# Optimization experiments

Measured on AMD Instinct MI355X. Metric: run time of the kernel, lower is better.

## Reference

```python
import jax, jax.numpy as jnp
import numpy as np

H = 128; W = 128; WH = 8; WW = 8; SH = 4; SW = 4
DIM = 512; HEADS = 16; HD = DIM // HEADS; HIDDEN = 2048
NH = H // WH; NW = W // WW; NWIN = NH * NW; WL = WH * WW
EPS = 1e-5
SCALE = HD ** -0.5


def _rel_pos_index():
    # Swin-style relative position index, static (WL, WL) int table
    coords = np.stack(np.meshgrid(np.arange(WH), np.arange(WW), indexing='ij')).reshape(2, -1)
    rel = (coords[:, :, None] - coords[:, None, :]).transpose(1, 2, 0)  # (WL, WL, 2)
    rel[:, :, 0] += WH - 1
    rel[:, :, 1] += WW - 1
    rel[:, :, 0] *= 2 * WW - 1
    return rel.sum(-1)  # (WL, WL), values in [0, (2WH-1)(2WW-1))


def _shift_attn_mask():
    # static shifted-window attention mask, (NWIN, WL, WL)
    m = np.zeros((H, W))
    cnt = 0
    for hs in (slice(0, -WH), slice(-WH, -SH), slice(-SH, None)):
        for ws in (slice(0, -WW), slice(-WW, -SW), slice(-SW, None)):
            m[hs, ws] = cnt
            cnt += 1
    mw = m.reshape(NH, WH, NW, WW).transpose(0, 2, 1, 3).reshape(NWIN, WL)
    am = mw[:, None, :] - mw[:, :, None]
    return np.where(am != 0, -100.0, 0.0).astype(np.float32)


_RPI = _rel_pos_index()
_MASK = _shift_attn_mask()


def _layernorm(x, w, b):
    mu = x.mean(-1, keepdims=True)
    var = ((x - mu) ** 2).mean(-1, keepdims=True)
    return (x - mu) / jnp.sqrt(var + EPS) * w + b


def _win_part(x):  # (H, W, D) -> (NWIN, WL, D)
    return x.reshape(NH, WH, NW, WW, DIM).transpose(0, 2, 1, 3, 4).reshape(NWIN, WL, DIM)


def _win_rev(w):  # (NWIN, WL, D) -> (H, W, D)
    return w.reshape(NH, NW, WH, WW, DIM).transpose(0, 2, 1, 3, 4).reshape(H, W, DIM)


def setup_inputs() -> dict:
    key = jax.random.key(0)
    ks = jax.random.split(key, 8)
    s = 0.02
    return {
        'x': jax.random.normal(ks[0], (H * W, DIM), dtype=jnp.float32),
        'ln1_w': jnp.ones((DIM,), jnp.float32),
        'ln1_b': jnp.zeros((DIM,), jnp.float32),
        'ln2_w': jnp.ones((DIM,), jnp.float32),
        'ln2_b': jnp.zeros((DIM,), jnp.float32),
        'qkv_w': jax.random.normal(ks[1], (3 * DIM, DIM), dtype=jnp.float32) * s,
        'qkv_b': jnp.zeros((3 * DIM,), jnp.float32),
        'proj_w': jax.random.normal(ks[2], (DIM, DIM), dtype=jnp.float32) * s,
        'proj_b': jnp.zeros((DIM,), jnp.float32),
        'rpb': jax.random.normal(ks[3], ((2 * WH - 1) * (2 * WW - 1), HEADS), dtype=jnp.float32) * s,
        'mlp_w1': jax.random.normal(ks[4], (HIDDEN, DIM), dtype=jnp.float32) * s,
        'mlp_b1': jnp.zeros((HIDDEN,), jnp.float32),
        'mlp_w2': jax.random.normal(ks[5], (DIM, HIDDEN), dtype=jnp.float32) * s,
        'mlp_b2': jnp.zeros((DIM,), jnp.float32),
    }


def reference(x, ln1_w, ln1_b, ln2_w, ln2_b, qkv_w, qkv_b, proj_w, proj_b, rpb,
              mlp_w1, mlp_b1, mlp_w2, mlp_b2):
    skip = x
    h = _layernorm(x, ln1_w, ln1_b).reshape(H, W, DIM)
    # cyclic shift + window partition
    h = jnp.roll(h, shift=(-SH, -SW), axis=(0, 1))
    xw = _win_part(h)  # (NWIN, WL, DIM)
    # windowed multi-head self-attention (equinox Linear: y = W @ x + b)
    qkv = jnp.einsum('nld,ed->nle', xw, qkv_w) + qkv_b
    q, k, v = [t.reshape(NWIN, WL, HEADS, HD).transpose(0, 2, 1, 3)
               for t in jnp.split(qkv, 3, axis=-1)]  # each (NWIN, HEADS, WL, HD)
    attn = jnp.einsum('nhqd,nhkd->nhqk', q * SCALE, k)
    bias = rpb[_RPI.reshape(-1)].reshape(WL, WL, HEADS).transpose(2, 0, 1)  # (HEADS, WL, WL)
    attn = attn + bias[None] + jnp.asarray(_MASK)[:, None]
    attn = jax.nn.softmax(attn, axis=-1)
    out = jnp.einsum('nhqk,nhkd->nhqd', attn, v).transpose(0, 2, 1, 3).reshape(NWIN, WL, DIM)
    out = jnp.einsum('nld,ed->nle', out, proj_w) + proj_b
    # window reverse + reverse cyclic shift
    h = jnp.roll(_win_rev(out), shift=(SH, SW), axis=(0, 1)).reshape(H * W, DIM)
    h = skip + h  # residual (drop_path is Identity at rate 0)
    # FFN branch (note: original code does x = x + drop_path(x), i.e. 2*mlp(norm2(.)))
    h = _layernorm(h, ln2_w, ln2_b)
    m = jax.nn.gelu(jnp.einsum('ld,ed->le', h, mlp_w1) + mlp_b1)
    m = jnp.einsum('le,de->ld', m, mlp_w2) + mlp_b2
    return m + m
```

## Files before the change

### kernel.cpp

```cpp
#include <hip/hip_runtime.h>
#include <hip/hip_bf16.h>
#include <stdint.h>

#define TOK   16384
#define DIMM  512
#define NHEAD 16
#define HDIM  32
#define HID   2048
#define NWIN  256
#define WLEN  64
#define EPSV  1e-5f
#define SCL   0.17677669529663687f

typedef __hip_bfloat16 bf16;
typedef __attribute__((ext_vector_type(8))) __bf16 bf16x8;
typedef __attribute__((ext_vector_type(4))) float f32x4;

__device__ __forceinline__ int remap_row(int r){
  int win = r >> 6, l = r & 63;
  int gh = ((win >> 4) << 3) + (l >> 3);
  int gw = ((win & 15) << 3) + (l & 7);
  int oh = (gh + 4) & 127, ow = (gw + 4) & 127;
  return (oh << 7) + ow;
}

__device__ __forceinline__ int region_of(int win, int l){
  int gh = ((win >> 4) << 3) + (l >> 3);
  int gw = ((win & 15) << 3) + (l & 7);
  int rh = (gh < 120) ? 0 : ((gh < 124) ? 1 : 2);
  int rw = (gw < 120) ? 0 : ((gw < 124) ? 1 : 2);
  return rh * 3 + rw;
}

__device__ __forceinline__ void gl_lds16(const bf16* g, bf16* l){
  __builtin_amdgcn_global_load_lds((const __attribute__((address_space(1))) void*)g,
                                   (__attribute__((address_space(3))) void*)l, 16, 0, 0);
}

__global__ __launch_bounds__(256) void convert_w(const float* __restrict__ a,
                                                 const float* __restrict__ b,
                                                 const float* __restrict__ c,
                                                 const float* __restrict__ d,
                                                 bf16* __restrict__ dst){
  int e = (blockIdx.x * 256 + threadIdx.x) * 4;
  float4 v;
  if (e < 786432)        v = *(const float4*)(a + e);
  else if (e < 1048576)  v = *(const float4*)(b + (e - 786432));
  else if (e < 2097152)  v = *(const float4*)(c + (e - 1048576));
  else                   v = *(const float4*)(d + (e - 2097152));
  union { bf16 h[4]; int2 q; } u;
  u.h[0] = __float2bfloat16(v.x); u.h[1] = __float2bfloat16(v.y);
  u.h[2] = __float2bfloat16(v.z); u.h[3] = __float2bfloat16(v.w);
  *(int2*)(dst + e) = u.q;
}

template<bool REMAP>
__global__ __launch_bounds__(256) void ln_kernel(const float* __restrict__ in,
    const float* __restrict__ w, const float* __restrict__ b, bf16* __restrict__ outp)
{
  const int wave = threadIdx.x >> 6, lane = threadIdx.x & 63;
  const int r = blockIdx.x * 4 + wave;
  const int src = REMAP ? remap_row(r) : r;
  const float4* row = (const float4*)(in + (size_t)src * DIMM);
  float4 v0 = row[lane*2], v1 = row[lane*2 + 1];
  float sm = v0.x+v0.y+v0.z+v0.w + v1.x+v1.y+v1.z+v1.w;
  float sq = v0.x*v0.x+v0.y*v0.y+v0.z*v0.z+v0.w*v0.w
           + v1.x*v1.x+v1.y*v1.y+v1.z*v1.z+v1.w*v1.w;
  #pragma unroll
  for (int off = 1; off < 64; off <<= 1){
    sm += __shfl_xor(sm, off);
    sq += __shfl_xor(sq, off);
  }
  const float mean = sm * (1.f/512.f);
  const float rstd = rsqrtf(sq*(1.f/512.f) - mean*mean + EPSV);
  const float4* wp = (const float4*)w; const float4* bp = (const float4*)b;
  float4 w0 = wp[lane*2], w1 = wp[lane*2+1], b0 = bp[lane*2], b1 = bp[lane*2+1];
  union { bf16 h[8]; int4 q; } u;
  u.h[0] = __float2bfloat16((v0.x-mean)*rstd*w0.x + b0.x);
  u.h[1] = __float2bfloat16((v0.y-mean)*rstd*w0.y + b0.y);
  u.h[2] = __float2bfloat16((v0.z-mean)*rstd*w0.z + b0.z);
  u.h[3] = __float2bfloat16((v0.w-mean)*rstd*w0.w + b0.w);
  u.h[4] = __float2bfloat16((v1.x-mean)*rstd*w1.x + b1.x);
  u.h[5] = __float2bfloat16((v1.y-mean)*rstd*w1.y + b1.y);
  u.h[6] = __float2bfloat16((v1.z-mean)*rstd*w1.z + b1.z);
  u.h[7] = __float2bfloat16((v1.w-mean)*rstd*w1.w + b1.w);
  *(int4*)(outp + (size_t)r*DIMM + lane*8) = u.q;
}

#define M_QKV  0
#define M_PROJ 1
#define M_MLP1 2
#define M_MLP2 3

template<int MODE, int K>
__global__ __launch_bounds__(256) void gemm_bt(const bf16* __restrict__ A,
    const bf16* __restrict__ Wt, const float* __restrict__ bias,
    bf16* __restrict__ out_b, float* __restrict__ out_f, const float* __restrict__ skip)
{
  __shared__ bf16 lsA[2][128*32];
  __shared__ bf16 lsB[2][128*32];
  const int tid = threadIdx.x, wave = tid >> 6, lane = tid & 63;
  const int lrow = lane & 15, lgrp = lane >> 4;
  const int m0 = blockIdx.x * 128, n0 = blockIdx.y * 128;
  const int wr = (wave >> 1) * 64, wc = (wave & 1) * 64;

  f32x4 acc[4][4] = {};

  const bf16* Abase = A  + (size_t)m0 * K;
  const bf16* Bbase = Wt + (size_t)n0 * K;
  const int srow = tid >> 2;
  const int scol = (tid & 3) * 8;

  #define STAGE(kt, bf) { \
    gl_lds16(Abase + (size_t)(srow)      * K + (kt) + scol, lsA[bf] + wave*512); \
    gl_lds16(Abase + (size_t)(srow + 64) * K + (kt) + scol, lsA[bf] + 2048 + wave*512); \
    gl_lds16(Bbase + (size_t)(srow)      * K + (kt) + scol, lsB[bf] + wave*512); \
    gl_lds16(Bbase + (size_t)(srow + 64) * K + (kt) + scol, lsB[bf] + 2048 + wave*512); \
  }

  STAGE(0, 0);
  __syncthreads();
  int cur = 0;
  for (int kt = 0; kt < K; kt += 32){
    if (kt + 32 < K) STAGE(kt + 32, cur ^ 1);
    bf16x8 af[4], bfv[4];
    #pragma unroll
    for (int i = 0; i < 4; i++){
      af[i]  = *(const bf16x8*)(lsA[cur] + (wr + i*16 + lrow)*32 + lgrp*8);
      bfv[i] = *(const bf16x8*)(lsB[cur] + (wc + i*16 + lrow)*32 + lgrp*8);
    }
    #pragma unroll
    for (int i = 0; i < 4; i++)
      #pragma unroll
      for (int j = 0; j < 4; j++)
        acc[i][j] = __builtin_amdgcn_mfma_f32_16x16x32_bf16(af[i], bfv[j], acc[i][j], 0, 0, 0);
    __syncthreads();
    cur ^= 1;
  }
  #undef STAGE

  #pragma unroll
  for (int i = 0; i < 4; i++){
    #pragma unroll
    for (int j = 0; j < 4; j++){
      const int col   = n0 + wc + j*16 + lrow;
      const int row_b = m0 + wr + i*16 + lgrp*4;
      const float bv = bias[col];
      #pragma unroll
      for (int rr = 0; rr < 4; rr++){
        const int row = row_b + rr;
        float v = acc[i][j][rr] + bv;
        if constexpr (MODE == M_QKV){
          const int t = col >> 9, rem = col & 511;
          const int head = rem >> 5, hd = rem & 31;
          const int win = row >> 6, l = row & 63;
          out_b[(size_t)t * (TOK*DIMM) + ((size_t)(win*NHEAD + head)*WLEN + l)*HDIM + hd]
              = __float2bfloat16(v);
        } else if constexpr (MODE == M_PROJ){
          const int o = remap_row(row);
          out_f[(size_t)o*DIMM + col] = v + skip[(size_t)o*DIMM + col];
        } else if constexpr (MODE == M_MLP1){
          const float u = 1.5957691216057308f * (v + 0.044715f*v*v*v);
          const float g = v * (1.0f / (1.0f + __expf(-u)));
          out_b[(size_t)row*HID + col] = __float2bfloat16(g);
        } else {
          out_f[(size_t)row*DIMM + col] = 2.f * v;
        }
      }
    }
  }
}

__global__ __launch_bounds__(256) void attn_kernel(const bf16* __restrict__ qkv,
    const float* __restrict__ rpb, bf16* __restrict__ outp)
{
  __shared__ bf16 Pl[4][64][72];
  const int wave = threadIdx.x >> 6, lane = threadIdx.x & 63;
  const int lrow = lane & 15, lgrp = lane >> 4;
  const int wh = blockIdx.x * 4 + wave;
  const int win = wh >> 4, head = wh & 15;
  const bf16* qb = qkv + (size_t)wh * (WLEN*HDIM);
  const bf16* kb = qb + (size_t)TOK * DIMM;
  const bf16* vb = kb + (size_t)TOK * DIMM;

  bf16x8 aq[4], ak[4];
  #pragma unroll
  for (int i = 0; i < 4; i++){
    aq[i] = *(const bf16x8*)(qb + (i*16 + lrow)*HDIM + lgrp*8);
    ak[i] = *(const bf16x8*)(kb + (i*16 + lrow)*HDIM + lgrp*8);
  }
  f32x4 s[4][4] = {};
  #pragma unroll
  for (int i = 0; i < 4; i++)
    #pragma unroll
    for (int j = 0; j < 4; j++)
      s[i][j] = __builtin_amdgcn_mfma_f32_16x16x32_bf16(aq[i], ak[j], s[i][j], 0, 0, 0);

  #pragma unroll
  for (int i = 0; i < 4; i++){
    #pragma unroll
    for (int rr = 0; rr < 4; rr++){
      const int srow = i*16 + lgrp*4 + rr;
      const int rq = region_of(win, srow);
      float vals[4]; float mx = -1e30f;
      #pragma unroll
      for (int j = 0; j < 4; j++){
        const int scol = j*16 + lrow;
        const int idx = ((srow>>3) - (scol>>3) + 7)*15 + ((srow&7) - (scol&7) + 7);
        float v = s[i][j][rr]*SCL + rpb[idx*NHEAD + head];
        if (region_of(win, scol) != rq) v -= 100.f;
        vals[j] = v; mx = fmaxf(mx, v);
      }
      mx = fmaxf(mx, __shfl_xor(mx, 1));
      mx = fmaxf(mx, __shfl_xor(mx, 2));
      mx = fmaxf(mx, __shfl_xor(mx, 4));
      mx = fmaxf(mx, __shfl_xor(mx, 8));
      float sum = 0.f;
      #pragma unroll
      for (int j = 0; j < 4; j++){ vals[j] = __expf(vals[j] - mx); sum += vals[j]; }
      sum += __shfl_xor(sum, 1); sum += __shfl_xor(sum, 2);
      sum += __shfl_xor(sum, 4); sum += __shfl_xor(sum, 8);
      const float rs = 1.f / sum;
      #pragma unroll
      for (int j = 0; j < 4; j++)
        Pl[wave][srow][j*16 + lrow] = __float2bfloat16(vals[j] * rs);
    }
  }

  f32x4 o[4][2] = {};
  const __bf16* vraw = (const __bf16*)vb;
  #pragma unroll
  for (int st = 0; st < 2; st++){
    bf16x8 pa[4];
    #pragma unroll
    for (int i = 0; i < 4; i++)
      pa[i] = *(const bf16x8*)(&Pl[wave][i*16 + lrow][st*32 + lgrp*8]);
    bf16x8 bv[2];
    #pragma unroll
    for (int j = 0; j < 2; j++){
      #pragma unroll
      for (int jj = 0; jj < 8; jj++)
        bv[j][jj] = vraw[(size_t)(st*32 + lgrp*8 + jj)*HDIM + j*16 + lrow];
    }
    #pragma unroll
    for (int i = 0; i < 4; i++)
      #pragma unroll
      for (int j = 0; j < 2; j++)
        o[i][j] = __builtin_amdgcn_mfma_f32_16x16x32_bf16(pa[i], bv[j], o[i][j], 0, 0, 0);
  }
  bf16* orow = outp + (size_t)win * WLEN * DIMM + head * HDIM;
  #pragma unroll
  for (int i = 0; i < 4; i++)
    #pragma unroll
    for (int j = 0; j < 2; j++)
      #pragma unroll
      for (int rr = 0; rr < 4; rr++){
        const int l = i*16 + lgrp*4 + rr;
        orow[(size_t)l * DIMM + j*16 + lrow] = __float2bfloat16(o[i][j][rr]);
      }
}

extern "C" void kernel_launch(void* const* d_in, const int* in_sizes, int n_in,
                              void* d_out, int out_size, void* d_ws, size_t ws_size,
                              hipStream_t stream) {
  const float* x     = (const float*)d_in[0];
  const float* ln1w  = (const float*)d_in[1];
  const float* ln1b  = (const float*)d_in[2];
  const float* ln2w  = (const float*)d_in[3];
  const float* ln2b  = (const float*)d_in[4];
  const float* qkvw  = (const float*)d_in[5];
  const float* qkvbi = (const float*)d_in[6];
  const float* projw = (const float*)d_in[7];
  const float* projb = (const float*)d_in[8];
  const float* rpb   = (const float*)d_in[9];
  const float* m1w   = (const float*)d_in[10];
  const float* m1b   = (const float*)d_in[11];
  const float* m2w   = (const float*)d_in[12];
  const float* m2b   = (const float*)d_in[13];

  bf16* wqkv  = (bf16*)d_ws;
  bf16* wproj = wqkv + 786432;
  bf16* wm1   = wproj + 262144;
  bf16* wm2   = wm1 + 1048576;
  bf16* xw    = wm2 + 1048576;
  float* hbuf = (float*)(xw + 8388608);
  bf16* qkvb  = (bf16*)(hbuf + 8388608);
  bf16* attno = qkvb + 3*(size_t)8388608;
  bf16* m1buf = qkvb;
  bf16* h2    = xw;

  convert_w<<<3072, 256, 0, stream>>>(qkvw, projw, m1w, m2w, wqkv);
  ln_kernel<true><<<4096, 256, 0, stream>>>(x, ln1w, ln1b, xw);
  { dim3 g(TOK/128, 1536/128);
    gemm_bt<M_QKV, 512><<<g, 256, 0, stream>>>(xw, wqkv, qkvbi, qkvb, nullptr, nullptr); }
  attn_kernel<<<1024, 256, 0, stream>>>(qkvb, rpb, attno);
  { dim3 g(TOK/128, 512/128);
    gemm_bt<M_PROJ, 512><<<g, 256, 0, stream>>>(attno, wproj, projb, nullptr, hbuf, x); }
  ln_kernel<false><<<4096, 256, 0, stream>>>(hbuf, ln2w, ln2b, h2);
  { dim3 g(TOK/128, 2048/128);
    gemm_bt<M_MLP1, 512><<<g, 256, 0, stream>>>(h2, wm1, m1b, m1buf, nullptr, nullptr); }
  { dim3 g(TOK/128, 512/128);
    gemm_bt<M_MLP2, 2048><<<g, 256, 0, stream>>>(m1buf, wm2, m2b, nullptr, (float*)d_out, nullptr); }
}
```

Before: 227.6 us.

## Add 256x256 eight-wave pipelined GEMM for QKV and MLP projections

Introduces a new GEMM kernel with 256x256 tiles, 512 threads (8 waves), double-buffered LDS staging via direct global-to-LDS loads, and an interleaved schedule that overlaps MFMA quadrants with LDS reads and next-tile prefetch using explicit barriers and priority hints. The QKV, MLP1 and MLP2 GEMMs now use it, while the proj GEMM keeps the old kernel, whose epilogue is trimmed to proj and generic modes. The larger tile raises arithmetic intensity and cuts global traffic. In exchange it uses 128KB of dynamic LDS and launches fewer blocks, which may hurt occupancy and tail balance, especially for MLP2 with 128 blocks.

```diff
diff --git a/kernel.cpp b/kernel.cpp
--- a/kernel.cpp
+++ b/kernel.cpp
@@ -150,15 +150,117 @@
       for (int rr = 0; rr < 4; rr++){
         const int row = row_b + rr;
         float v = acc[i][j][rr] + bv;
+        if constexpr (MODE == M_PROJ){
+          const int o = remap_row(row);
+          out_f[(size_t)o*DIMM + col] = v + skip[(size_t)o*DIMM + col];
+        } else {
+          out_f[(size_t)row*DIMM + col] = v;
+        }
+      }
+    }
+  }
+}
+
+__device__ __forceinline__ void stage_ht(const bf16* __restrict__ P, int Kdim,
+                                         int grow0, bf16* lbase, int tid, int kt){
+  const int r = tid >> 3, c = (tid & 7) * 8;
+  const bf16* g = P + (size_t)(grow0 + r) * Kdim + kt * 64 + c;
+  bf16* l = lbase + r * 64 + c;
+  gl_lds16(g, l);
+  gl_lds16(g + (size_t)64 * Kdim, l + 4096);
+}
+
+template<int MODE, int K>
+__global__ __launch_bounds__(512, 2) void gemm8_bt(const bf16* __restrict__ A,
+    const bf16* __restrict__ Wt, const float* __restrict__ bias,
+    bf16* __restrict__ out_b, float* __restrict__ out_f)
+{
+  constexpr int NT = K / 64;
+  extern __shared__ bf16 lds[];
+  bf16* As = lds;
+  bf16* Bs = lds + 32768;
+  const int tid = threadIdx.x;
+  const int ln = tid & 63, wv = tid >> 6;
+  const int lrow = ln & 15, lgrp = ln >> 4;
+  const int wm = wv >> 2, wn = wv & 3;
+  const int m0 = blockIdx.x * 256, n0 = blockIdx.y * 256;
+
+  f32x4 acc[8][4] = {};
+  bf16x8 aA[4][2], bB0[2][2], bB1[2][2];
+
+  #define LDA(MH) { _Pragma("unroll") for (int mf = 0; mf < 4; mf++) \
+    _Pragma("unroll") for (int ks = 0; ks < 2; ks++) \
+      aA[mf][ks] = *(const bf16x8*)(As + s*16384 + (wm*128 + (MH)*64 + mf*16 + lrow)*64 + ks*32 + lgrp*8); }
+  #define LDB(DST, NH) { _Pragma("unroll") for (int nf = 0; nf < 2; nf++) \
+    _Pragma("unroll") for (int ks = 0; ks < 2; ks++) \
+      DST[nf][ks] = *(const bf16x8*)(Bs + s*16384 + (wn*64 + (NH)*32 + nf*16 + lrow)*64 + ks*32 + lgrp*8); }
+  #define QUAD(BARR, IM0, JN0) { _Pragma("unroll") for (int ks = 0; ks < 2; ks++) \
+    _Pragma("unroll") for (int mf = 0; mf < 4; mf++) \
+      _Pragma("unroll") for (int nf = 0; nf < 2; nf++) \
+        acc[(IM0)+mf][(JN0)+nf] = __builtin_amdgcn_mfma_f32_16x16x32_bf16(aA[mf][ks], BARR[nf][ks], acc[(IM0)+mf][(JN0)+nf], 0, 0, 0); }
+  #define SBAR() { __builtin_amdgcn_sched_barrier(0); __builtin_amdgcn_s_barrier(); __builtin_amdgcn_sched_barrier(0); }
+  #define LGKM0() { asm volatile("s_waitcnt lgkmcnt(0)" ::: "memory"); __builtin_amdgcn_sched_barrier(0); }
+
+  stage_ht(A,  K, m0,       As,        tid, 0);
+  stage_ht(Wt, K, n0,       Bs,        tid, 0);
+  stage_ht(Wt, K, n0 + 128, Bs + 8192, tid, 0);
+  stage_ht(A,  K, m0 + 128, As + 8192, tid, 0);
+  asm volatile("s_waitcnt vmcnt(0)" ::: "memory");
+  SBAR();
+  stage_ht(Wt, K, n0,       Bs + 16384,        tid, 1);
+  stage_ht(A,  K, m0,       As + 16384,        tid, 1);
+  stage_ht(Wt, K, n0 + 128, Bs + 16384 + 8192, tid, 1);
+
+  for (int t = 0; t < NT; ++t){
+    const int s = t & 1;
+    const int sx = s ^ 1;
+    LDA(0); LDB(bB0, 0);
+    if (t + 1 < NT) stage_ht(A, K, m0 + 128, As + sx*16384 + 8192, tid, t + 1);
+    SBAR(); LGKM0();
+    __builtin_amdgcn_s_setprio(1); QUAD(bB0, 0, 0); __builtin_amdgcn_s_setprio(0);
+    SBAR();
+    LDB(bB1, 1);
+    SBAR(); LGKM0();
+    __builtin_amdgcn_s_setprio(1); QUAD(bB1, 0, 2); __builtin_amdgcn_s_setprio(0);
+    SBAR();
+    LDA(1);
+    if (t + 2 < NT) stage_ht(Wt, K, n0, Bs + s*16384, tid, t + 2);
+    SBAR(); LGKM0();
+    __builtin_amdgcn_s_setprio(1); QUAD(bB1, 4, 2); __builtin_amdgcn_s_setprio(0);
+    SBAR();
+    if (t + 2 < NT){
+      stage_ht(A,  K, m0,       As + s*16384,        tid, t + 2);
+      stage_ht(Wt, K, n0 + 128, Bs + s*16384 + 8192, tid, t + 2);
+    }
+    SBAR();
+    __builtin_amdgcn_s_setprio(1); QUAD(bB0, 4, 0); __builtin_amdgcn_s_setprio(0);
+    if (t == NT - 2)      { asm volatile("s_waitcnt vmcnt(0)" ::: "memory"); }
+    else if (t < NT - 2)  { asm volatile("s_waitcnt vmcnt(6)" ::: "memory"); }
+    SBAR();
+  }
+  #undef LDA
+  #undef LDB
+  #undef QUAD
+  #undef SBAR
+  #undef LGKM0
+
+  #pragma unroll
+  for (int im = 0; im < 8; im++){
+    #pragma unroll
+    for (int jn = 0; jn < 4; jn++){
+      const int col = n0 + wn*64 + (jn >> 1)*32 + (jn & 1)*16 + lrow;
+      const int row_b = m0 + wm*128 + (im >> 2)*64 + (im & 3)*16 + lgrp*4;
+      const float bv = bias[col];
+      #pragma unroll
+      for (int rr = 0; rr < 4; rr++){
+        const int row = row_b + rr;
+        float v = acc[im][jn][rr] + bv;
         if constexpr (MODE == M_QKV){
           const int t = col >> 9, rem = col & 511;
           const int head = rem >> 5, hd = rem & 31;
           const int win = row >> 6, l = row & 63;
           out_b[(size_t)t * (TOK*DIMM) + ((size_t)(win*NHEAD + head)*WLEN + l)*HDIM + hd]
               = __float2bfloat16(v);
-        } else if constexpr (MODE == M_PROJ){
-          const int o = remap_row(row);
-          out_f[(size_t)o*DIMM + col] = v + skip[(size_t)o*DIMM + col];
         } else if constexpr (MODE == M_MLP1){
           const float u = 1.5957691216057308f * (v + 0.044715f*v*v*v);
           const float g = v * (1.0f / (1.0f + __expf(-u)));
@@ -289,16 +391,23 @@
   bf16* m1buf = qkvb;
   bf16* h2    = xw;
 
+  hipFuncSetAttribute((const void*)&gemm8_bt<M_QKV, 512>,
+                      hipFuncAttributeMaxDynamicSharedMemorySize, 131072);
+  hipFuncSetAttribute((const void*)&gemm8_bt<M_MLP1, 512>,
+                      hipFuncAttributeMaxDynamicSharedMemorySize, 131072);
+  hipFuncSetAttribute((const void*)&gemm8_bt<M_MLP2, 2048>,
+                      hipFuncAttributeMaxDynamicSharedMemorySize, 131072);
+
   convert_w<<<3072, 256, 0, stream>>>(qkvw, projw, m1w, m2w, wqkv);
   ln_kernel<true><<<4096, 256, 0, stream>>>(x, ln1w, ln1b, xw);
-  { dim3 g(TOK/128, 1536/128);
-    gemm_bt<M_QKV, 512><<<g, 256, 0, stream>>>(xw, wqkv, qkvbi, qkvb, nullptr, nullptr); }
+  { dim3 g(TOK/256, 1536/256);
+    gemm8_bt<M_QKV, 512><<<g, 512, 131072, stream>>>(xw, wqkv, qkvbi, qkvb, nullptr); }
   attn_kernel<<<1024, 256, 0, stream>>>(qkvb, rpb, attno);
   { dim3 g(TOK/128, 512/128);
     gemm_bt<M_PROJ, 512><<<g, 256, 0, stream>>>(attno, wproj, projb, nullptr, hbuf, x); }
   ln_kernel<false><<<4096, 256, 0, stream>>>(hbuf, ln2w, ln2b, h2);
-  { dim3 g(TOK/128, 2048/128);
-    gemm_bt<M_MLP1, 512><<<g, 256, 0, stream>>>(h2, wm1, m1b, m1buf, nullptr, nullptr); }
-  { dim3 g(TOK/128, 512/128);
-    gemm_bt<M_MLP2, 2048><<<g, 256, 0, stream>>>(m1buf, wm2, m2b, nullptr, (float*)d_out, nullptr); }
-}
+  { dim3 g(TOK/256, 2048/256);
+    gemm8_bt<M_MLP1, 512><<<g, 512, 131072, stream>>>(h2, wm1, m1b, m1buf, nullptr); }
+  { dim3 g(TOK/256, 512/256);
+    gemm8_bt<M_MLP2, 2048><<<g, 512, 131072, stream>>>(m1buf, wm2, m2b, nullptr, (float*)d_out); }
+}
```

After: 269.9 us. +18.5%, slower.

## Add 128x256-tile 512-thread GEMM kernel for QKV and MLP GEMMs

Applied to the files above, without the earlier changes.

Adds a new GEMM kernel using 128x256 output tiles with 8 waves, each computing 64x64. It double-buffers via direct global-to-LDS loads with an XOR-swizzled layout. QKV, MLP1 and MLP2 now use this kernel, while the projection GEMM stays on the original kernel, whose epilogue is trimmed to the proj case. The larger N tile raises A-operand reuse and halves the grid along N, at the cost of more LDS per block and fewer blocks for the small-N MLP2 GEMM.

```diff
diff --git a/kernel.cpp b/kernel.cpp
--- a/kernel.cpp
+++ b/kernel.cpp
@@ -150,15 +150,86 @@
       for (int rr = 0; rr < 4; rr++){
         const int row = row_b + rr;
         float v = acc[i][j][rr] + bv;
+        if constexpr (MODE == M_PROJ){
+          const int o = remap_row(row);
+          out_f[(size_t)o*DIMM + col] = v + skip[(size_t)o*DIMM + col];
+        } else {
+          out_f[(size_t)row*DIMM + col] = v;
+        }
+      }
+    }
+  }
+}
+
+template<int MODE, int K>
+__global__ __launch_bounds__(512, 4) void gemm_a(const bf16* __restrict__ A,
+    const bf16* __restrict__ Wt, const float* __restrict__ bias,
+    bf16* __restrict__ out_b, float* __restrict__ out_f)
+{
+  constexpr int NT = K / 32;
+  __shared__ bf16 As[2][128*32];
+  __shared__ bf16 Bs[2][256*32];
+  const int tid = threadIdx.x;
+  const int ln = tid & 63, wv = tid >> 6;
+  const int lrow = ln & 15, lgrp = ln >> 4;
+  const int wm = wv >> 2, wn = wv & 3;
+  const int m0 = blockIdx.x * 128, n0 = blockIdx.y * 256;
+
+  f32x4 acc[4][4] = {};
+
+  const int sr = tid >> 2;
+  const int sc = ((tid & 3) ^ ((sr >> 1) & 3)) * 8;
+  const int sd = sr * 32 + (tid & 3) * 8;
+  const bf16* Ab  = A  + (size_t)(m0 + sr) * K + sc;
+  const bf16* Bb0 = Wt + (size_t)(n0 + sr) * K + sc;
+  const bf16* Bb1 = Wt + (size_t)(n0 + 128 + sr) * K + sc;
+
+  #define STAGE(kt, sl) { \
+    gl_lds16(Ab  + (kt)*32, &As[sl][sd]); \
+    gl_lds16(Bb0 + (kt)*32, &Bs[sl][sd]); \
+    gl_lds16(Bb1 + (kt)*32, &Bs[sl][4096 + sd]); \
+  }
+
+  const int rswz = (lgrp ^ ((lrow >> 1) & 3)) * 8;
+
+  STAGE(0, 0);
+  __syncthreads();
+  for (int kt = 0; kt < NT; ++kt){
+    const int s = kt & 1;
+    if (kt + 1 < NT) STAGE(kt + 1, s ^ 1);
+    bf16x8 a[4], b[4];
+    #pragma unroll
+    for (int mf = 0; mf < 4; mf++)
+      a[mf] = *(const bf16x8*)(&As[s][(wm*64 + mf*16 + lrow)*32 + rswz]);
+    #pragma unroll
+    for (int nf = 0; nf < 4; nf++)
+      b[nf] = *(const bf16x8*)(&Bs[s][(wn*64 + nf*16 + lrow)*32 + rswz]);
+    #pragma unroll
+    for (int mf = 0; mf < 4; mf++)
+      #pragma unroll
+      for (int nf = 0; nf < 4; nf++)
+        acc[mf][nf] = __builtin_amdgcn_mfma_f32_16x16x32_bf16(a[mf], b[nf], acc[mf][nf], 0, 0, 0);
+    __syncthreads();
+  }
+  #undef STAGE
+
+  #pragma unroll
+  for (int mf = 0; mf < 4; mf++){
+    #pragma unroll
+    for (int nf = 0; nf < 4; nf++){
+      const int col = n0 + wn*64 + nf*16 + lrow;
+      const int row_b = m0 + wm*64 + mf*16 + lgrp*4;
+      const float bv = bias[col];
+      #pragma unroll
+      for (int rr = 0; rr < 4; rr++){
+        const int row = row_b + rr;
+        float v = acc[mf][nf][rr] + bv;
         if constexpr (MODE == M_QKV){
           const int t = col >> 9, rem = col & 511;
           const int head = rem >> 5, hd = rem & 31;
           const int win = row >> 6, l = row & 63;
           out_b[(size_t)t * (TOK*DIMM) + ((size_t)(win*NHEAD + head)*WLEN + l)*HDIM + hd]
               = __float2bfloat16(v);
-        } else if constexpr (MODE == M_PROJ){
-          const int o = remap_row(row);
-          out_f[(size_t)o*DIMM + col] = v + skip[(size_t)o*DIMM + col];
         } else if constexpr (MODE == M_MLP1){
           const float u = 1.5957691216057308f * (v + 0.044715f*v*v*v);
           const float g = v * (1.0f / (1.0f + __expf(-u)));
@@ -291,14 +362,14 @@
 
   convert_w<<<3072, 256, 0, stream>>>(qkvw, projw, m1w, m2w, wqkv);
   ln_kernel<true><<<4096, 256, 0, stream>>>(x, ln1w, ln1b, xw);
-  { dim3 g(TOK/128, 1536/128);
-    gemm_bt<M_QKV, 512><<<g, 256, 0, stream>>>(xw, wqkv, qkvbi, qkvb, nullptr, nullptr); }
+  { dim3 g(TOK/128, 1536/256);
+    gemm_a<M_QKV, 512><<<g, 512, 0, stream>>>(xw, wqkv, qkvbi, qkvb, nullptr); }
   attn_kernel<<<1024, 256, 0, stream>>>(qkvb, rpb, attno);
   { dim3 g(TOK/128, 512/128);
     gemm_bt<M_PROJ, 512><<<g, 256, 0, stream>>>(attno, wproj, projb, nullptr, hbuf, x); }
   ln_kernel<false><<<4096, 256, 0, stream>>>(hbuf, ln2w, ln2b, h2);
-  { dim3 g(TOK/128, 2048/128);
-    gemm_bt<M_MLP1, 512><<<g, 256, 0, stream>>>(h2, wm1, m1b, m1buf, nullptr, nullptr); }
-  { dim3 g(TOK/128, 512/128);
-    gemm_bt<M_MLP2, 2048><<<g, 256, 0, stream>>>(m1buf, wm2, m2b, nullptr, (float*)d_out, nullptr); }
-}
+  { dim3 g(TOK/128, 2048/256);
+    gemm_a<M_MLP1, 512><<<g, 512, 0, stream>>>(h2, wm1, m1b, m1buf, nullptr); }
+  { dim3 g(TOK/128, 512/256);
+    gemm_a<M_MLP2, 2048><<<g, 512, 0, stream>>>(m1buf, wm2, m2b, nullptr, (float*)d_out); }
+}
```

Result: no change. 227.3 us (-0.1%).

## Rewrite GEMMs with 256x256 tiles, 32x32 MFMA and XOR-swizzled LDS

Applied to the files above, without the earlier changes.

Replaces the 128x128 GEMM with a 256x256 block tile, a BK=64 double-buffered stage of 128KB dynamic LDS, and 32x32x16 MFMA instructions. An XOR swizzle on the LDS layout is meant to avoid bank conflicts. The goal is more operand reuse per loaded byte and fewer LDS reads per FLOP. In exchange, each CU runs only one block, and the grids become small: 64x2 blocks for the proj and MLP2 GEMMs, which may leave CUs idle on a 256-CU part.

```diff
diff --git a/kernel.cpp b/kernel.cpp
--- a/kernel.cpp
+++ b/kernel.cpp
@@ -15,6 +15,7 @@
 typedef __hip_bfloat16 bf16;
 typedef __attribute__((ext_vector_type(8))) __bf16 bf16x8;
 typedef __attribute__((ext_vector_type(4))) float f32x4;
+typedef __attribute__((ext_vector_type(16))) float f32x16;
 
 __device__ __forceinline__ int remap_row(int r){
   int win = r >> 6, l = r & 63;
@@ -93,63 +94,64 @@
 #define M_MLP2 3
 
 template<int MODE, int K>
-__global__ __launch_bounds__(256) void gemm_bt(const bf16* __restrict__ A,
+__global__ __launch_bounds__(256, 1) void gemm_c(const bf16* __restrict__ A,
     const bf16* __restrict__ Wt, const float* __restrict__ bias,
     bf16* __restrict__ out_b, float* __restrict__ out_f, const float* __restrict__ skip)
 {
-  __shared__ bf16 lsA[2][128*32];
-  __shared__ bf16 lsB[2][128*32];
-  const int tid = threadIdx.x, wave = tid >> 6, lane = tid & 63;
-  const int lrow = lane & 15, lgrp = lane >> 4;
-  const int m0 = blockIdx.x * 128, n0 = blockIdx.y * 128;
-  const int wr = (wave >> 1) * 64, wc = (wave & 1) * 64;
-
-  f32x4 acc[4][4] = {};
-
-  const bf16* Abase = A  + (size_t)m0 * K;
-  const bf16* Bbase = Wt + (size_t)n0 * K;
-  const int srow = tid >> 2;
-  const int scol = (tid & 3) * 8;
-
-  #define STAGE(kt, bf) { \
-    gl_lds16(Abase + (size_t)(srow)      * K + (kt) + scol, lsA[bf] + wave*512); \
-    gl_lds16(Abase + (size_t)(srow + 64) * K + (kt) + scol, lsA[bf] + 2048 + wave*512); \
-    gl_lds16(Bbase + (size_t)(srow)      * K + (kt) + scol, lsB[bf] + wave*512); \
-    gl_lds16(Bbase + (size_t)(srow + 64) * K + (kt) + scol, lsB[bf] + 2048 + wave*512); \
-  }
+  constexpr int NT = K / 64;
+  extern __shared__ bf16 lds[];
+  bf16* As = lds;
+  bf16* Bs = lds + 32768;
+  const int tid = threadIdx.x, lane = tid & 63, wv = tid >> 6;
+  const int wm = wv >> 1, wn = wv & 1;
+  const int l31 = lane & 31, lg2 = lane >> 5, l7 = lane & 7;
+  const int m0 = blockIdx.x * 256, n0 = blockIdx.y * 256;
+
+  f32x16 acc[4][4] = {};
+
+  const int srow   = wv*8 + (lane >> 3);
+  const int schunk = l7 ^ (lane >> 3);
+  const int sdest  = wv*8*64 + lane*8;
+
+  #define STAGE(kt, sl) { _Pragma("unroll") for (int i = 0; i < 8; i++){ \
+    gl_lds16(A  + (size_t)(m0 + i*32 + srow)*K + (kt)*64 + schunk*8, As + (sl)*16384 + i*2048 + sdest); \
+    gl_lds16(Wt + (size_t)(n0 + i*32 + srow)*K + (kt)*64 + schunk*8, Bs + (sl)*16384 + i*2048 + sdest); } }
 
   STAGE(0, 0);
   __syncthreads();
-  int cur = 0;
-  for (int kt = 0; kt < K; kt += 32){
-    if (kt + 32 < K) STAGE(kt + 32, cur ^ 1);
-    bf16x8 af[4], bfv[4];
-    #pragma unroll
-    for (int i = 0; i < 4; i++){
-      af[i]  = *(const bf16x8*)(lsA[cur] + (wr + i*16 + lrow)*32 + lgrp*8);
-      bfv[i] = *(const bf16x8*)(lsB[cur] + (wc + i*16 + lrow)*32 + lgrp*8);
+  for (int kt = 0; kt < NT; ++kt){
+    const int s = kt & 1;
+    if (kt + 1 < NT) STAGE(kt + 1, s ^ 1);
+    #pragma unroll
+    for (int ks = 0; ks < 4; ks++){
+      const int pc = ((ks*2 + lg2) ^ l7) * 8;
+      bf16x8 a[4], b[4];
+      #pragma unroll
+      for (int mf = 0; mf < 4; mf++)
+        a[mf] = *(const bf16x8*)(As + s*16384 + (wm*128 + mf*32 + l31)*64 + pc);
+      #pragma unroll
+      for (int nf = 0; nf < 4; nf++)
+        b[nf] = *(const bf16x8*)(Bs + s*16384 + (wn*128 + nf*32 + l31)*64 + pc);
+      #pragma unroll
+      for (int mf = 0; mf < 4; mf++)
+        #pragma unroll
+        for (int nf = 0; nf < 4; nf++)
+          acc[mf][nf] = __builtin_amdgcn_mfma_f32_32x32x16_bf16(a[mf], b[nf], acc[mf][nf], 0, 0, 0);
     }
-    #pragma unroll
-    for (int i = 0; i < 4; i++)
-      #pragma unroll
-      for (int j = 0; j < 4; j++)
-        acc[i][j] = __builtin_amdgcn_mfma_f32_16x16x32_bf16(af[i], bfv[j], acc[i][j], 0, 0, 0);
     __syncthreads();
-    cur ^= 1;
   }
   #undef STAGE
 
   #pragma unroll
-  for (int i = 0; i < 4; i++){
-    #pragma unroll
-    for (int j = 0; j < 4; j++){
-      const int col   = n0 + wc + j*16 + lrow;
-      const int row_b = m0 + wr + i*16 + lgrp*4;
+  for (int mf = 0; mf < 4; mf++){
+    #pragma unroll
+    for (int nf = 0; nf < 4; nf++){
+      const int col = n0 + wn*128 + nf*32 + l31;
       const float bv = bias[col];
       #pragma unroll
-      for (int rr = 0; rr < 4; rr++){
-        const int row = row_b + rr;
-        float v = acc[i][j][rr] + bv;
+      for (int reg = 0; reg < 16; reg++){
+        const int row = m0 + wm*128 + mf*32 + (reg & 3) + ((reg >> 2) << 3) + lg2*4;
+        float v = acc[mf][nf][reg] + bv;
         if constexpr (MODE == M_QKV){
           const int t = col >> 9, rem = col & 511;
           const int head = rem >> 5, hd = rem & 31;
@@ -289,16 +291,25 @@
   bf16* m1buf = qkvb;
   bf16* h2    = xw;
 
+  hipFuncSetAttribute((const void*)&gemm_c<M_QKV, 512>,
+                      hipFuncAttributeMaxDynamicSharedMemorySize, 131072);
+  hipFuncSetAttribute((const void*)&gemm_c<M_PROJ, 512>,
+                      hipFuncAttributeMaxDynamicSharedMemorySize, 131072);
+  hipFuncSetAttribute((const void*)&gemm_c<M_MLP1, 512>,
+                      hipFuncAttributeMaxDynamicSharedMemorySize, 131072);
+  hipFuncSetAttribute((const void*)&gemm_c<M_MLP2, 2048>,
+                      hipFuncAttributeMaxDynamicSharedMemorySize, 131072);
+
   convert_w<<<3072, 256, 0, stream>>>(qkvw, projw, m1w, m2w, wqkv);
   ln_kernel<true><<<4096, 256, 0, stream>>>(x, ln1w, ln1b, xw);
-  { dim3 g(TOK/128, 1536/128);
-    gemm_bt<M_QKV, 512><<<g, 256, 0, stream>>>(xw, wqkv, qkvbi, qkvb, nullptr, nullptr); }
+  { dim3 g(TOK/256, 1536/256);
+    gemm_c<M_QKV, 512><<<g, 256, 131072, stream>>>(xw, wqkv, qkvbi, qkvb, nullptr, nullptr); }
   attn_kernel<<<1024, 256, 0, stream>>>(qkvb, rpb, attno);
-  { dim3 g(TOK/128, 512/128);
-    gemm_bt<M_PROJ, 512><<<g, 256, 0, stream>>>(attno, wproj, projb, nullptr, hbuf, x); }
+  { dim3 g(TOK/256, 512/256);
+    gemm_c<M_PROJ, 512><<<g, 256, 131072, stream>>>(attno, wproj, projb, nullptr, hbuf, x); }
   ln_kernel<false><<<4096, 256, 0, stream>>>(hbuf, ln2w, ln2b, h2);
-  { dim3 g(TOK/128, 2048/128);
-    gemm_bt<M_MLP1, 512><<<g, 256, 0, stream>>>(h2, wm1, m1b, m1buf, nullptr, nullptr); }
-  { dim3 g(TOK/128, 512/128);
-    gemm_bt<M_MLP2, 2048><<<g, 256, 0, stream>>>(m1buf, wm2, m2b, nullptr, (float*)d_out, nullptr); }
-}
+  { dim3 g(TOK/256, 2048/256);
+    gemm_c<M_MLP1, 512><<<g, 256, 131072, stream>>>(h2, wm1, m1b, m1buf, nullptr, nullptr); }
+  { dim3 g(TOK/256, 512/256);
+    gemm_c<M_MLP2, 2048><<<g, 256, 131072, stream>>>(m1buf, wm2, m2b, nullptr, (float*)d_out, nullptr); }
+}
```

New measurement: 242.4 us. 1.06x slower.
